# Kernel tuning notes

Measured on AMD Instinct MI355X. Metric: run time of the kernel, lower is better.

The kernel has to match this reference:

```python
import jax, jax.numpy as jnp
import numpy as np

B, L, D, V = 512, 128, 512, 100000

def setup_inputs() -> dict:
    key = jax.random.key(0)
    ks = jax.random.split(key, 8)
    return {
        "t1s": jax.random.randint(ks[0], (B,), 0, V),
        "t2s": jax.random.randint(ks[1], (B,), 0, V),
        "t1_contexts": jax.random.randint(ks[2], (B, L), 0, V),
        "t2_contexts": jax.random.randint(ks[3], (B, L), 0, V),
        "embed_table": jax.random.normal(ks[4], (V, D), dtype=jnp.float32),
        "att_mat": jax.random.normal(ks[5], (D, D), dtype=jnp.float32) * (6.0 / (D + D)) ** 0.5,
        "w_pred": jax.random.normal(ks[6], (D, 1), dtype=jnp.float32) * 0.02,
        "b_pred": jnp.zeros((1,), dtype=jnp.float32),
    }

def _frob_normalize(x):
    # torch.norm(mat, p=2) is the Frobenius norm of the whole (L, D) matrix
    n = jnp.sqrt(jnp.sum(x * x, axis=(1, 2), keepdims=True))
    return x / n

def reference(t1s, t2s, t1_contexts, t2_contexts, embed_table, att_mat, w_pred, b_pred):
    # dropout is identity in eval mode; t1s/t2s embeddings are unused in the
    # 'dynamic' branch (dead code in the original forward).
    A = _frob_normalize(embed_table[t1_contexts])  # (B, L, D)
    Bm = _frob_normalize(embed_table[t2_contexts])  # (B, L, D)
    # batched bilinear attention: tanh(A @ att_mat @ B^T)
    S = jnp.tanh(jnp.einsum('bld,de,bme->blm', A, att_mat, Bm))  # (B, L, L)
    rows = jax.nn.softmax(jnp.mean(S, axis=2), axis=1)  # (B, L)
    cols = jax.nn.softmax(jnp.mean(S, axis=1), axis=1)  # (B, L)
    newA = jnp.einsum('bld,bl->bd', A, rows)   # (B, D)
    newB = jnp.einsum('bld,bl->bd', Bm, cols)  # (B, D)
    logits = ((newA * newB) @ w_pred + b_pred).reshape(-1)  # (B,)
    return logits, S
```

## Files before the change

kernel.cpp:

```cpp
#include <hip/hip_runtime.h>
#include <hip/hip_bf16.h>
#include <stdint.h>

#define NB 512
#define NL 128
#define ND 512

typedef __bf16 bf16;
typedef __bf16 bf16x8 __attribute__((ext_vector_type(8)));
typedef float  f32x4  __attribute__((ext_vector_type(4)));

#define GLDS(src, dst) __builtin_amdgcn_global_load_lds( \
    (const __attribute__((address_space(1))) void*)(src), \
    (__attribute__((address_space(3))) void*)(dst), 16, 0, 0)

__global__ __launch_bounds__(256) void k_gather(const int* __restrict__ ctx1,
                                                const int* __restrict__ ctx2,
                                                const float* __restrict__ table,
                                                bf16* __restrict__ d1,
                                                bf16* __restrict__ d2,
                                                float* __restrict__ ss,
                                                const float* __restrict__ att,
                                                bf16* __restrict__ attT) {
    const int b = blockIdx.x, side = blockIdx.y, zc = blockIdx.z, t = threadIdx.x;
    if (side == 2) {
        int chunk = b * 8 + zc;
        if (chunk < 1024) {
            int i = chunk * 256 + t;
            int n = i >> 9, k = i & 511;
            attT[i] = (bf16)att[k * 512 + n];
        }
        return;
    }
    const int* __restrict__ ctx = side ? ctx2 : ctx1;
    bf16* __restrict__ dst = side ? d2 : d1;
    const int base = b * NL;
    const int dv = t & 127, lr = t >> 7;
    int idxs[8];
    #pragma unroll
    for (int i = 0; i < 8; ++i) idxs[i] = ctx[base + zc * 16 + i * 2 + lr];
    float acc = 0.f;
    #pragma unroll
    for (int i = 0; i < 8; ++i) {
        int l = zc * 16 + i * 2 + lr;
        float4 v = ((const float4*)table)[(size_t)idxs[i] * (ND / 4) + dv];
        acc += v.x * v.x + v.y * v.y + v.z * v.z + v.w * v.w;
        union { bf16 h[4]; uint2 u; } pk;
        pk.h[0] = (bf16)v.x; pk.h[1] = (bf16)v.y;
        pk.h[2] = (bf16)v.z; pk.h[3] = (bf16)v.w;
        *((uint2*)(dst + (size_t)(base + l) * ND) + dv) = pk.u;
    }
    for (int o = 32; o; o >>= 1) acc += __shfl_xor(acc, o);
    __shared__ float red[4];
    if ((t & 63) == 0) red[t >> 6] = acc;
    __syncthreads();
    if (t == 0) atomicAdd(&ss[side * NB + b], red[0] + red[1] + red[2] + red[3]);
}

__global__ __launch_bounds__(512) void k_fused(
        const bf16* __restrict__ Ab, const bf16* __restrict__ attT,
        const bf16* __restrict__ Bb, float* __restrict__ Sout,
        const float* __restrict__ ss,
        const float* __restrict__ w_pred, const float* __restrict__ b_pred,
        float* __restrict__ logits) {
    const int b = blockIdx.x;
    const int row0 = b * NL;
    const int tid = threadIdx.x;
    const int lane = tid & 63, w = tid >> 6;
    const int lm = lane & 15, quad = lane >> 4;

    __shared__ __align__(16) char smem[151552];
    bf16* sA0 = (bf16*)smem;
    bf16* sT0 = (bf16*)(smem + 8192);
    bf16* sA1 = (bf16*)(smem + 40960);
    bf16* sT1 = (bf16*)(smem + 49152);
    bf16* Tls = (bf16*)smem;
    bf16* sB0 = (bf16*)(smem + 131072);
    bf16* sB1 = (bf16*)(smem + 139264);
    float* pA = (float*)smem;
    float* pB = (float*)(smem + 16384);
    float* rowb = (float*)(smem + 147456);
    float* colb = (float*)(smem + 147456 + 2048);
    float* wrow = (float*)(smem + 147456 + 3072);
    float* wcol = (float*)(smem + 147456 + 3584);

    const int wm1 = (w & 1) * 64;
    const int wn1 = (w >> 1) * 128;
    f32x4 acc1[4][8] = {};

    const int rA = tid >> 2, cA = tid & 3;

    GLDS(Ab + (size_t)(row0 + rA) * ND + 0 + cA * 8, sA0 + tid * 8);
    #pragma unroll
    for (int i = 0; i < 4; ++i) {
        int s = i * 512 + tid, r = s >> 2, c = s & 3;
        GLDS(attT + (size_t)r * ND + 0 + c * 8, sT0 + s * 8);
    }
    __syncthreads();

    for (int t = 0; t < 16; ++t) {
        if (t < 15) {
            const int k0 = (t + 1) * 32;
            bf16* dA = (t & 1) ? sA0 : sA1;
            bf16* dT = (t & 1) ? sT0 : sT1;
            GLDS(Ab + (size_t)(row0 + rA) * ND + k0 + cA * 8, dA + tid * 8);
            #pragma unroll
            for (int i = 0; i < 4; ++i) {
                int s = i * 512 + tid, r = s >> 2, c = s & 3;
                GLDS(attT + (size_t)r * ND + k0 + c * 8, dT + s * 8);
            }
        } else {
            GLDS(Bb + (size_t)(row0 + rA) * ND + 0 + cA * 8, sB0 + tid * 8);
        }
        const bf16* A_ = (t & 1) ? sA1 : sA0;
        const bf16* T_ = (t & 1) ? sT1 : sT0;
        bf16x8 af[4], bfm[8];
        #pragma unroll
        for (int t4 = 0; t4 < 4; ++t4)
            af[t4] = *(const bf16x8*)&A_[(wm1 + t4 * 16 + lm) * 32 + quad * 8];
        #pragma unroll
        for (int t8 = 0; t8 < 8; ++t8)
            bfm[t8] = *(const bf16x8*)&T_[(wn1 + t8 * 16 + lm) * 32 + quad * 8];
        #pragma unroll
        for (int im = 0; im < 4; ++im)
            #pragma unroll
            for (int jn = 0; jn < 8; ++jn)
                acc1[im][jn] = __builtin_amdgcn_mfma_f32_16x16x32_bf16(
                    af[im], bfm[jn], acc1[im][jn], 0, 0, 0);
        __syncthreads();
    }

    #pragma unroll
    for (int im = 0; im < 4; ++im)
    #pragma unroll
    for (int jn = 0; jn < 8; ++jn)
    #pragma unroll
    for (int p = 0; p < 4; ++p) {
        int m = wm1 + im * 16 + quad * 4 + p;
        int n = wn1 + jn * 16 + lm;
        int ks = n >> 5, kq = (n >> 3) & 3, e = n & 7;
        int pos = kq ^ ((m >> 2) & 3);
        Tls[ks * 4096 + m * 32 + pos * 8 + e] = (bf16)acc1[im][jn][p];
    }
    __syncthreads();

    const int wm2 = (w & 1) * 64;
    const int wn2 = (w >> 1) * 32;
    f32x4 acc2[4][2] = {};

    for (int t = 0; t < 16; ++t) {
        if (t < 15) {
            bf16* dB = (t & 1) ? sB0 : sB1;
            GLDS(Bb + (size_t)(row0 + rA) * ND + (t + 1) * 32 + cA * 8, dB + tid * 8);
        }
        const bf16* B_ = (t & 1) ? sB1 : sB0;
        bf16x8 af[4], bf2[2];
        #pragma unroll
        for (int t4 = 0; t4 < 4; ++t4) {
            int r = wm2 + t4 * 16 + lm;
            af[t4] = *(const bf16x8*)&Tls[t * 4096 + r * 32 + ((quad ^ ((r >> 2) & 3))) * 8];
        }
        #pragma unroll
        for (int t2 = 0; t2 < 2; ++t2)
            bf2[t2] = *(const bf16x8*)&B_[(wn2 + t2 * 16 + lm) * 32 + quad * 8];
        #pragma unroll
        for (int im = 0; im < 4; ++im)
            #pragma unroll
            for (int jn = 0; jn < 2; ++jn)
                acc2[im][jn] = __builtin_amdgcn_mfma_f32_16x16x32_bf16(
                    af[im], bf2[jn], acc2[im][jn], 0, 0, 0);
        __syncthreads();
    }

    const float sc = rsqrtf(ss[b] * ss[NB + b]);
    float* __restrict__ Sb = Sout + (size_t)b * NL * NL;
    #pragma unroll
    for (int im = 0; im < 4; ++im)
    #pragma unroll
    for (int jn = 0; jn < 2; ++jn)
    #pragma unroll
    for (int p = 0; p < 4; ++p) {
        float v = tanhf(acc2[im][jn][p] * sc);
        acc2[im][jn][p] = v;
        int m = wm2 + im * 16 + quad * 4 + p;
        int n = wn2 + jn * 16 + lm;
        __builtin_nontemporal_store(v, &Sb[m * NL + n]);
    }
    #pragma unroll
    for (int im = 0; im < 4; ++im)
    #pragma unroll
    for (int p = 0; p < 4; ++p) {
        float r = acc2[im][0][p] + acc2[im][1][p];
        r += __shfl_xor(r, 1); r += __shfl_xor(r, 2);
        r += __shfl_xor(r, 4); r += __shfl_xor(r, 8);
        if (lm == 0) rowb[(w >> 1) * NL + wm2 + im * 16 + quad * 4 + p] = r;
    }
    #pragma unroll
    for (int jn = 0; jn < 2; ++jn) {
        float cv = 0.f;
        #pragma unroll
        for (int im = 0; im < 4; ++im)
            #pragma unroll
            for (int p = 0; p < 4; ++p) cv += acc2[im][jn][p];
        cv += __shfl_xor(cv, 16); cv += __shfl_xor(cv, 32);
        if (quad == 0) colb[(w & 1) * NL + wn2 + jn * 16 + lm] = cv;
    }
    __syncthreads();

    if (tid < 64) {
        float a  = (rowb[0 * NL + tid] + rowb[1 * NL + tid] + rowb[2 * NL + tid] + rowb[3 * NL + tid]) * (1.f / NL);
        float c2 = (rowb[0 * NL + tid + 64] + rowb[1 * NL + tid + 64] + rowb[2 * NL + tid + 64] + rowb[3 * NL + tid + 64]) * (1.f / NL);
        float mx = fmaxf(a, c2);
        for (int o = 32; o; o >>= 1) mx = fmaxf(mx, __shfl_xor(mx, o));
        float e0 = expf(a - mx), e1 = expf(c2 - mx);
        float s = e0 + e1;
        for (int o = 32; o; o >>= 1) s += __shfl_xor(s, o);
        float inv = 1.f / s;
        wrow[tid] = e0 * inv; wrow[tid + 64] = e1 * inv;
    } else if (tid < 128) {
        int q = tid - 64;
        float a  = (colb[0 * NL + q] + colb[1 * NL + q]) * (1.f / NL);
        float c2 = (colb[0 * NL + q + 64] + colb[1 * NL + q + 64]) * (1.f / NL);
        float mx = fmaxf(a, c2);
        for (int o = 32; o; o >>= 1) mx = fmaxf(mx, __shfl_xor(mx, o));
        float e0 = expf(a - mx), e1 = expf(c2 - mx);
        float s = e0 + e1;
        for (int o = 32; o; o >>= 1) s += __shfl_xor(s, o);
        float inv = 1.f / s;
        wcol[q] = e0 * inv; wcol[q + 64] = e1 * inv;
    }
    __syncthreads();

    const int c = tid & 63, g = tid >> 6;
    const bf16* __restrict__ Abase = Ab + (size_t)b * NL * ND;
    const bf16* __restrict__ Bbase = Bb + (size_t)b * NL * ND;
    float aacc[8] = {}, bacc[8] = {};
    for (int l = g; l < NL; l += 8) {
        float wr = wrow[l], wc = wcol[l];
        bf16x8 va = *(const bf16x8*)(Abase + (size_t)l * ND + c * 8);
        bf16x8 vb = *(const bf16x8*)(Bbase + (size_t)l * ND + c * 8);
        #pragma unroll
        for (int j = 0; j < 8; ++j) {
            aacc[j] += wr * (float)va[j];
            bacc[j] += wc * (float)vb[j];
        }
    }
    #pragma unroll
    for (int j = 0; j < 8; ++j) {
        pA[g * ND + c * 8 + j] = aacc[j];
        pB[g * ND + c * 8 + j] = bacc[j];
    }
    __syncthreads();

    if (tid < 64) {
        float dot = 0.f;
        #pragma unroll
        for (int j = 0; j < 8; ++j) {
            int d = tid * 8 + j;
            float na = 0.f, nb = 0.f;
            #pragma unroll
            for (int g2 = 0; g2 < 8; ++g2) {
                na += pA[g2 * ND + d];
                nb += pB[g2 * ND + d];
            }
            dot += na * nb * w_pred[d];
        }
        for (int o = 32; o; o >>= 1) dot += __shfl_xor(dot, o);
        if (tid == 0)
            logits[b] = dot * rsqrtf(ss[b]) * rsqrtf(ss[NB + b]) + b_pred[0];
    }
}

extern "C" void kernel_launch(void* const* d_in, const int* in_sizes, int n_in,
                              void* d_out, int out_size, void* d_ws, size_t ws_size,
                              hipStream_t stream) {
    const int*   t1c = (const int*)d_in[2];
    const int*   t2c = (const int*)d_in[3];
    const float* emb = (const float*)d_in[4];
    const float* att = (const float*)d_in[5];
    const float* wp  = (const float*)d_in[6];
    const float* bp  = (const float*)d_in[7];

    float* out    = (float*)d_out;
    float* logits = out;
    float* S      = out + NB;

    char* ws = (char*)d_ws;
    bf16*  Ab   = (bf16*)(ws);
    bf16*  Bb   = (bf16*)(ws + 67108864);
    bf16*  attT = (bf16*)(ws + 134217728);
    float* ss   = (float*)(ws + 134742016);

    hipMemsetAsync(ss, 0, 4096, stream);
    k_gather<<<dim3(NB, 3, 8), 256, 0, stream>>>(t1c, t2c, emb, Ab, Bb, ss, att, attT);
    k_fused<<<dim3(NB), 512, 0, stream>>>(Ab, attT, Bb, S, ss, wp, bp, logits);
}
```

Before: 406.8 us.

## Fuse embedding gather into main kernel and compute logits via weighted Gram MFMA

The separate gather kernel and the memset are removed. Each block of the main kernel now gathers its own A and B context rows, converts them to bf16, and computes the Frobenius norms locally, so no atomics are needed. The final weighted-sum pass over A and B is replaced by an extra MFMA accumulation of A·diag(w_pred)·Bᵀ, run alongside the second GEMM and then reduced with the row and column softmax weights. This saves one launch and a full reread of A and B. In exchange the gather now runs with one large-LDS block per CU and less parallelism, and the second GEMM loop does twice the MFMA work plus extra LDS traffic.

```diff
diff --git a/kernel.cpp b/kernel.cpp
--- a/kernel.cpp
+++ b/kernel.cpp
@@ -14,87 +14,80 @@
     (const __attribute__((address_space(1))) void*)(src), \
     (__attribute__((address_space(3))) void*)(dst), 16, 0, 0)
 
-__global__ __launch_bounds__(256) void k_gather(const int* __restrict__ ctx1,
-                                                const int* __restrict__ ctx2,
-                                                const float* __restrict__ table,
-                                                bf16* __restrict__ d1,
-                                                bf16* __restrict__ d2,
-                                                float* __restrict__ ss,
-                                                const float* __restrict__ att,
-                                                bf16* __restrict__ attT) {
-    const int b = blockIdx.x, side = blockIdx.y, zc = blockIdx.z, t = threadIdx.x;
-    if (side == 2) {
-        int chunk = b * 8 + zc;
-        if (chunk < 1024) {
-            int i = chunk * 256 + t;
-            int n = i >> 9, k = i & 511;
-            attT[i] = (bf16)att[k * 512 + n];
-        }
-        return;
-    }
-    const int* __restrict__ ctx = side ? ctx2 : ctx1;
-    bf16* __restrict__ dst = side ? d2 : d1;
-    const int base = b * NL;
-    const int dv = t & 127, lr = t >> 7;
-    int idxs[8];
-    #pragma unroll
-    for (int i = 0; i < 8; ++i) idxs[i] = ctx[base + zc * 16 + i * 2 + lr];
-    float acc = 0.f;
-    #pragma unroll
-    for (int i = 0; i < 8; ++i) {
-        int l = zc * 16 + i * 2 + lr;
-        float4 v = ((const float4*)table)[(size_t)idxs[i] * (ND / 4) + dv];
-        acc += v.x * v.x + v.y * v.y + v.z * v.z + v.w * v.w;
-        union { bf16 h[4]; uint2 u; } pk;
-        pk.h[0] = (bf16)v.x; pk.h[1] = (bf16)v.y;
-        pk.h[2] = (bf16)v.z; pk.h[3] = (bf16)v.w;
-        *((uint2*)(dst + (size_t)(base + l) * ND) + dv) = pk.u;
-    }
-    for (int o = 32; o; o >>= 1) acc += __shfl_xor(acc, o);
-    __shared__ float red[4];
-    if ((t & 63) == 0) red[t >> 6] = acc;
-    __syncthreads();
-    if (t == 0) atomicAdd(&ss[side * NB + b], red[0] + red[1] + red[2] + red[3]);
+__global__ __launch_bounds__(256) void k_attT(const float* __restrict__ att,
+                                              bf16* __restrict__ attT) {
+    int i = blockIdx.x * 256 + threadIdx.x;
+    int n = i >> 9, k = i & 511;
+    attT[i] = (bf16)att[k * 512 + n];
 }
 
-__global__ __launch_bounds__(512) void k_fused(
-        const bf16* __restrict__ Ab, const bf16* __restrict__ attT,
-        const bf16* __restrict__ Bb, float* __restrict__ Sout,
-        const float* __restrict__ ss,
-        const float* __restrict__ w_pred, const float* __restrict__ b_pred,
-        float* __restrict__ logits) {
-    const int b = blockIdx.x;
-    const int row0 = b * NL;
-    const int tid = threadIdx.x;
+__global__ __launch_bounds__(512) void k_mega(
+        const int* __restrict__ ctx1, const int* __restrict__ ctx2,
+        const float* __restrict__ table, const bf16* __restrict__ attT,
+        bf16* __restrict__ Ab, bf16* __restrict__ Bb,
+        float* __restrict__ Sout, const float* __restrict__ w_pred,
+        const float* __restrict__ b_pred, float* __restrict__ logits) {
+    const int b = blockIdx.x, row0 = b * NL, tid = threadIdx.x;
     const int lane = tid & 63, w = tid >> 6;
     const int lm = lane & 15, quad = lane >> 4;
 
-    __shared__ __align__(16) char smem[151552];
+    __shared__ __align__(16) char smem[163840];
     bf16* sA0 = (bf16*)smem;
-    bf16* sT0 = (bf16*)(smem + 8192);
-    bf16* sA1 = (bf16*)(smem + 40960);
+    bf16* sA1 = (bf16*)(smem + 8192);
+    bf16* sT0 = (bf16*)(smem + 16384);
     bf16* sT1 = (bf16*)(smem + 49152);
     bf16* Tls = (bf16*)smem;
     bf16* sB0 = (bf16*)(smem + 131072);
     bf16* sB1 = (bf16*)(smem + 139264);
-    float* pA = (float*)smem;
-    float* pB = (float*)(smem + 16384);
-    float* rowb = (float*)(smem + 147456);
-    float* colb = (float*)(smem + 147456 + 2048);
-    float* wrow = (float*)(smem + 147456 + 3072);
-    float* wcol = (float*)(smem + 147456 + 3584);
+    bf16* sC0 = (bf16*)(smem + 147456);
+    bf16* sC1 = (bf16*)(smem + 155648);
+    float* red  = (float*)(smem + 1024);
+    float* rowb = (float*)smem;
+    float* colb = (float*)(smem + 2048);
+    float* wrow = (float*)(smem + 3072);
+    float* wcol = (float*)(smem + 3584);
+    float* red2 = (float*)(smem + 2048);
+
+    const int r8 = tid >> 6, c8 = tid & 63;
+    float pa = 0.f, pb = 0.f;
+    #pragma unroll 4
+    for (int j = 0; j < 16; ++j) {
+        int l = j * 8 + r8;
+        int ia = ctx1[row0 + l], ib = ctx2[row0 + l];
+        const float4* ra = (const float4*)table + (size_t)ia * (ND / 4) + c8 * 2;
+        const float4* rb = (const float4*)table + (size_t)ib * (ND / 4) + c8 * 2;
+        float4 a0 = ra[0], a1 = ra[1];
+        float4 b0 = rb[0], b1 = rb[1];
+        pa += a0.x*a0.x + a0.y*a0.y + a0.z*a0.z + a0.w*a0.w
+            + a1.x*a1.x + a1.y*a1.y + a1.z*a1.z + a1.w*a1.w;
+        pb += b0.x*b0.x + b0.y*b0.y + b0.z*b0.z + b0.w*b0.w
+            + b1.x*b1.x + b1.y*b1.y + b1.z*b1.z + b1.w*b1.w;
+        union { bf16 h[8]; uint4 u; } ua, ub;
+        ua.h[0]=(bf16)a0.x; ua.h[1]=(bf16)a0.y; ua.h[2]=(bf16)a0.z; ua.h[3]=(bf16)a0.w;
+        ua.h[4]=(bf16)a1.x; ua.h[5]=(bf16)a1.y; ua.h[6]=(bf16)a1.z; ua.h[7]=(bf16)a1.w;
+        ub.h[0]=(bf16)b0.x; ub.h[1]=(bf16)b0.y; ub.h[2]=(bf16)b0.z; ub.h[3]=(bf16)b0.w;
+        ub.h[4]=(bf16)b1.x; ub.h[5]=(bf16)b1.y; ub.h[6]=(bf16)b1.z; ub.h[7]=(bf16)b1.w;
+        *(uint4*)(Ab + (size_t)(row0 + l) * ND + c8 * 8) = ua.u;
+        *(uint4*)(Bb + (size_t)(row0 + l) * ND + c8 * 8) = ub.u;
+    }
+    for (int o = 32; o; o >>= 1) { pa += __shfl_xor(pa, o); pb += __shfl_xor(pb, o); }
+    if (lane == 0) { red[w * 2] = pa; red[w * 2 + 1] = pb; }
+    __syncthreads();
+    float ssA = 0.f, ssB = 0.f;
+    #pragma unroll
+    for (int i = 0; i < 8; ++i) { ssA += red[i * 2]; ssB += red[i * 2 + 1]; }
+    __syncthreads();
 
     const int wm1 = (w & 1) * 64;
     const int wn1 = (w >> 1) * 128;
     f32x4 acc1[4][8] = {};
-
     const int rA = tid >> 2, cA = tid & 3;
 
-    GLDS(Ab + (size_t)(row0 + rA) * ND + 0 + cA * 8, sA0 + tid * 8);
+    GLDS(Ab + (size_t)(row0 + rA) * ND + cA * 8, sA0 + tid * 8);
     #pragma unroll
     for (int i = 0; i < 4; ++i) {
         int s = i * 512 + tid, r = s >> 2, c = s & 3;
-        GLDS(attT + (size_t)r * ND + 0 + c * 8, sT0 + s * 8);
+        GLDS(attT + (size_t)r * ND + c * 8, sT0 + s * 8);
     }
     __syncthreads();
 
@@ -110,7 +103,8 @@
                 GLDS(attT + (size_t)r * ND + k0 + c * 8, dT + s * 8);
             }
         } else {
-            GLDS(Bb + (size_t)(row0 + rA) * ND + 0 + cA * 8, sB0 + tid * 8);
+            GLDS(Bb + (size_t)(row0 + rA) * ND + cA * 8, sB0 + tid * 8);
+            GLDS(Ab + (size_t)(row0 + rA) * ND + cA * 8, sC0 + tid * 8);
         }
         const bf16* A_ = (t & 1) ? sA1 : sA0;
         const bf16* T_ = (t & 1) ? sT1 : sT0;
@@ -146,33 +140,47 @@
 
     const int wm2 = (w & 1) * 64;
     const int wn2 = (w >> 1) * 32;
-    f32x4 acc2[4][2] = {};
+    f32x4 acc2[4][2] = {}, accG[4][2] = {};
 
     for (int t = 0; t < 16; ++t) {
         if (t < 15) {
             bf16* dB = (t & 1) ? sB0 : sB1;
+            bf16* dC = (t & 1) ? sC0 : sC1;
             GLDS(Bb + (size_t)(row0 + rA) * ND + (t + 1) * 32 + cA * 8, dB + tid * 8);
+            GLDS(Ab + (size_t)(row0 + rA) * ND + (t + 1) * 32 + cA * 8, dC + tid * 8);
         }
         const bf16* B_ = (t & 1) ? sB1 : sB0;
-        bf16x8 af[4], bf2[2];
+        const bf16* C_ = (t & 1) ? sC1 : sC0;
+        float4 w0 = *(const float4*)(w_pred + t * 32 + quad * 8);
+        float4 w1 = *(const float4*)(w_pred + t * 32 + quad * 8 + 4);
+        float wv[8] = {w0.x, w0.y, w0.z, w0.w, w1.x, w1.y, w1.z, w1.w};
+        bf16x8 af[4], af2[4], bf2[2], bfw[2];
         #pragma unroll
         for (int t4 = 0; t4 < 4; ++t4) {
             int r = wm2 + t4 * 16 + lm;
-            af[t4] = *(const bf16x8*)&Tls[t * 4096 + r * 32 + ((quad ^ ((r >> 2) & 3))) * 8];
-        }
-        #pragma unroll
-        for (int t2 = 0; t2 < 2; ++t2)
+            af[t4]  = *(const bf16x8*)&Tls[t * 4096 + r * 32 + ((quad ^ ((r >> 2) & 3))) * 8];
+            af2[t4] = *(const bf16x8*)&C_[r * 32 + quad * 8];
+        }
+        #pragma unroll
+        for (int t2 = 0; t2 < 2; ++t2) {
             bf2[t2] = *(const bf16x8*)&B_[(wn2 + t2 * 16 + lm) * 32 + quad * 8];
+            #pragma unroll
+            for (int j = 0; j < 8; ++j)
+                bfw[t2][j] = (bf16)((float)bf2[t2][j] * wv[j]);
+        }
         #pragma unroll
         for (int im = 0; im < 4; ++im)
             #pragma unroll
-            for (int jn = 0; jn < 2; ++jn)
+            for (int jn = 0; jn < 2; ++jn) {
                 acc2[im][jn] = __builtin_amdgcn_mfma_f32_16x16x32_bf16(
                     af[im], bf2[jn], acc2[im][jn], 0, 0, 0);
+                accG[im][jn] = __builtin_amdgcn_mfma_f32_16x16x32_bf16(
+                    af2[im], bfw[jn], accG[im][jn], 0, 0, 0);
+            }
         __syncthreads();
     }
 
-    const float sc = rsqrtf(ss[b] * ss[NB + b]);
+    const float sc = rsqrtf(ssA * ssB);
     float* __restrict__ Sb = Sout + (size_t)b * NL * NL;
     #pragma unroll
     for (int im = 0; im < 4; ++im)
@@ -208,8 +216,8 @@
     __syncthreads();
 
     if (tid < 64) {
-        float a  = (rowb[0 * NL + tid] + rowb[1 * NL + tid] + rowb[2 * NL + tid] + rowb[3 * NL + tid]) * (1.f / NL);
-        float c2 = (rowb[0 * NL + tid + 64] + rowb[1 * NL + tid + 64] + rowb[2 * NL + tid + 64] + rowb[3 * NL + tid + 64]) * (1.f / NL);
+        float a  = (rowb[tid] + rowb[NL + tid] + rowb[2 * NL + tid] + rowb[3 * NL + tid]) * (1.f / NL);
+        float c2 = (rowb[tid + 64] + rowb[NL + tid + 64] + rowb[2 * NL + tid + 64] + rowb[3 * NL + tid + 64]) * (1.f / NL);
         float mx = fmaxf(a, c2);
         for (int o = 32; o; o >>= 1) mx = fmaxf(mx, __shfl_xor(mx, o));
         float e0 = expf(a - mx), e1 = expf(c2 - mx);
@@ -219,8 +227,8 @@
         wrow[tid] = e0 * inv; wrow[tid + 64] = e1 * inv;
     } else if (tid < 128) {
         int q = tid - 64;
-        float a  = (colb[0 * NL + q] + colb[1 * NL + q]) * (1.f / NL);
-        float c2 = (colb[0 * NL + q + 64] + colb[1 * NL + q + 64]) * (1.f / NL);
+        float a  = (colb[q] + colb[NL + q]) * (1.f / NL);
+        float c2 = (colb[q + 64] + colb[NL + q + 64]) * (1.f / NL);
         float mx = fmaxf(a, c2);
         for (int o = 32; o; o >>= 1) mx = fmaxf(mx, __shfl_xor(mx, o));
         float e0 = expf(a - mx), e1 = expf(c2 - mx);
@@ -231,43 +239,23 @@
     }
     __syncthreads();
 
-    const int c = tid & 63, g = tid >> 6;
-    const bf16* __restrict__ Abase = Ab + (size_t)b * NL * ND;
-    const bf16* __restrict__ Bbase = Bb + (size_t)b * NL * ND;
-    float aacc[8] = {}, bacc[8] = {};
-    for (int l = g; l < NL; l += 8) {
-        float wr = wrow[l], wc = wcol[l];
-        bf16x8 va = *(const bf16x8*)(Abase + (size_t)l * ND + c * 8);
-        bf16x8 vb = *(const bf16x8*)(Bbase + (size_t)l * ND + c * 8);
-        #pragma unroll
-        for (int j = 0; j < 8; ++j) {
-            aacc[j] += wr * (float)va[j];
-            bacc[j] += wc * (float)vb[j];
-        }
-    }
-    #pragma unroll
-    for (int j = 0; j < 8; ++j) {
-        pA[g * ND + c * 8 + j] = aacc[j];
-        pB[g * ND + c * 8 + j] = bacc[j];
-    }
-    __syncthreads();
-
-    if (tid < 64) {
-        float dot = 0.f;
-        #pragma unroll
-        for (int j = 0; j < 8; ++j) {
-            int d = tid * 8 + j;
-            float na = 0.f, nb = 0.f;
-            #pragma unroll
-            for (int g2 = 0; g2 < 8; ++g2) {
-                na += pA[g2 * ND + d];
-                nb += pB[g2 * ND + d];
-            }
-            dot += na * nb * w_pred[d];
-        }
-        for (int o = 32; o; o >>= 1) dot += __shfl_xor(dot, o);
-        if (tid == 0)
-            logits[b] = dot * rsqrtf(ss[b]) * rsqrtf(ss[NB + b]) + b_pred[0];
+    float wc0 = wcol[wn2 + lm], wc1 = wcol[wn2 + 16 + lm];
+    float g = 0.f;
+    #pragma unroll
+    for (int im = 0; im < 4; ++im)
+    #pragma unroll
+    for (int p = 0; p < 4; ++p) {
+        float wr = wrow[wm2 + im * 16 + quad * 4 + p];
+        g += wr * (wc0 * accG[im][0][p] + wc1 * accG[im][1][p]);
+    }
+    for (int o = 32; o; o >>= 1) g += __shfl_xor(g, o);
+    if (lane == 0) red2[w] = g;
+    __syncthreads();
+    if (tid == 0) {
+        float tot = 0.f;
+        #pragma unroll
+        for (int i = 0; i < 8; ++i) tot += red2[i];
+        logits[b] = tot * sc + b_pred[0];
     }
 }
 
@@ -289,9 +277,8 @@
     bf16*  Ab   = (bf16*)(ws);
     bf16*  Bb   = (bf16*)(ws + 67108864);
     bf16*  attT = (bf16*)(ws + 134217728);
-    float* ss   = (float*)(ws + 134742016);
-
-    hipMemsetAsync(ss, 0, 4096, stream);
-    k_gather<<<dim3(NB, 3, 8), 256, 0, stream>>>(t1c, t2c, emb, Ab, Bb, ss, att, attT);
-    k_fused<<<dim3(NB), 512, 0, stream>>>(Ab, attT, Bb, S, ss, wp, bp, logits);
+
+    k_attT<<<dim3(1024), 256, 0, stream>>>(att, attT);
+    k_mega<<<dim3(NB), 512, 0, stream>>>(t1c, t2c, emb, attT, Ab, Bb,
+                                         S, wp, bp, logits);
 }
```

New measurement: 387.8 us. -4.7%, faster.
